# Kernel tuning notes

Measured on AMD Instinct MI355X. Metric: run time of the kernel, lower is better.

## Reference

```python
import math
import jax, jax.numpy as jnp
import numpy as np

B, C, E = 8, 2048, 1024

def setup_inputs() -> dict:
    key = jax.random.key(0)
    ks = jax.random.split(key, 7)
    s_e = 1.0 / math.sqrt(E)
    s_c = 1.0 / math.sqrt(C)
    return {
        'x': jax.random.normal(ks[0], (B, C, E), dtype=jnp.float32),
        'fc_w': jax.random.normal(ks[1], (E, E), dtype=jnp.float32) * s_e,
        'fc_b': jax.random.normal(ks[2], (E,), dtype=jnp.float32) * s_e,
        'alt_fc_w': jax.random.normal(ks[3], (C, C), dtype=jnp.float32) * s_c,
        'alt_fc_b': jax.random.normal(ks[4], (C,), dtype=jnp.float32) * s_c,
        'vfc_w': jax.random.normal(ks[5], (E, E), dtype=jnp.float32) * s_e,
        'vfc_b': jax.random.normal(ks[6], (E,), dtype=jnp.float32) * s_e,
    }

def reference(x, fc_w, fc_b, alt_fc_w, alt_fc_b, vfc_w, vfc_b):
    # y = fc(x): [b,c,e]
    y = jnp.einsum('bce,fe->bcf', x, fc_w) + fc_b
    # yx = alt_fc(x^T): [b,e,c] -> Linear over context dim -> [b,e,k]
    xx = jnp.swapaxes(x, 1, 2)                    # [b,e,c]
    yx = jnp.einsum('bec,kc->bek', xx, alt_fc_w) + alt_fc_b
    # attention scores: [b,c,k]
    attn = jnp.einsum('bce,bek->bck', y, yx)
    scale = 1.0 / math.sqrt(attn.shape[-1])
    attn = jax.nn.softmax(attn * scale, axis=-1)
    # values
    vx = jnp.einsum('bke,fe->bkf', x, vfc_w) + vfc_b
    out = jnp.einsum('bck,bke->bce', attn, vx)
    # post_feed=None -> return y only
    return out
```

## Files before the change

### kernel.cpp

```cpp
#include <hip/hip_runtime.h>
#include <stdint.h>

#define Bb 8
#define Cc 2048
#define Ee 1024

typedef unsigned short u16;
typedef __attribute__((ext_vector_type(8))) short short8;
typedef __attribute__((ext_vector_type(4))) float f32x4;

__device__ __forceinline__ u16 f2bf(float f){
    unsigned u = __builtin_bit_cast(unsigned, f);
    return (u16)((u + 0x7fffu + ((u >> 16) & 1u)) >> 16);
}
__device__ __forceinline__ float bf2f(u16 h){
    return __builtin_bit_cast(float, ((unsigned)h) << 16);
}
__device__ __forceinline__ void gld16(const void* g, void* l){
    __builtin_amdgcn_global_load_lds(
        (const __attribute__((address_space(1))) unsigned int*)g,
        (__attribute__((address_space(3))) unsigned int*)l,
        16, 0, 0);
}
#define MFMA(a,b,c) __builtin_amdgcn_mfma_f32_16x16x32_bf16((a),(b),(c),0,0,0)
#define SBAR()  __builtin_amdgcn_s_barrier()
#define SCHED0() __builtin_amdgcn_sched_barrier(0)
#define LGKM8() asm volatile("s_waitcnt lgkmcnt(8)" ::: "memory")
#define LGKM0() asm volatile("s_waitcnt lgkmcnt(0)" ::: "memory")
#define VMCNT0() asm volatile("s_waitcnt vmcnt(0)" ::: "memory")

__global__ __launch_bounds__(256) void k_cast(const float* __restrict__ s,
                                              u16* __restrict__ d, long n4){
    long i = (long)blockIdx.x * 256 + threadIdx.x;
    const long stride = (long)gridDim.x * 256;
    for (; i < n4; i += stride){
        float4 f = ((const float4*)s)[i];
        ushort4 o = make_ushort4(f2bf(f.x), f2bf(f.y), f2bf(f.z), f2bf(f.w));
        ((ushort4*)d)[i] = o;
    }
}

__global__ __launch_bounds__(256) void k_cast_xt(const float* __restrict__ src,
                                                 u16* __restrict__ xb,
                                                 u16* __restrict__ xbT){
    __shared__ float tile[32][33];
    const int b = blockIdx.z;
    src += (long)b * Cc * Ee;
    xb  += (long)b * Cc * Ee;
    xbT += (long)b * Cc * Ee;
    const int c0 = blockIdx.x * 32;
    const int r0 = blockIdx.y * 32;
    const int tx = threadIdx.x & 31;
    const int ty = threadIdx.x >> 5;
    #pragma unroll
    for (int p = 0; p < 4; ++p){
        float v = src[(long)(r0 + ty + p*8) * Ee + c0 + tx];
        tile[ty + p*8][tx] = v;
        xb[(long)(r0 + ty + p*8) * Ee + c0 + tx] = f2bf(v);
    }
    __syncthreads();
    #pragma unroll
    for (int p = 0; p < 4; ++p)
        xbT[(long)(c0 + ty + p*8) * Cc + r0 + tx] = f2bf(tile[tx][ty + p*8]);
}

template<int BIAS_MODE, int OUT_F32>
__global__ __launch_bounds__(256, 2)
void k_gemm128(const u16* __restrict__ A, const u16* __restrict__ Bm,
               void* __restrict__ Cout, const float* __restrict__ bias,
               int N, int K, long sA, long sB, long sC, float scale)
{
    __shared__ __attribute__((aligned(16))) char smem[65536];

    const int gx = gridDim.x, gy = gridDim.y;
    const int nwg = gx * gy * gridDim.z;
    const int lin = blockIdx.x + gx * (blockIdx.y + gy * blockIdx.z);
    const int swz = (lin & 7) * (nwg >> 3) + (lin >> 3);
    const int bx = swz % gx;
    const int tmp = swz / gx;
    const int by = tmp % gy;
    const int bz = tmp / gy;

    A  += (long)bz * sA;
    Bm += (long)bz * sB;
    u16*   Cm = (u16*)Cout + (OUT_F32 ? 0 : (long)bz * sC);
    float* Cf = (float*)Cout + (OUT_F32 ? (long)bz * sC : 0);

    const int tid  = threadIdx.x;
    const int lane = tid & 63;
    const int wave = tid >> 6;
    const int wr = wave >> 1;
    const int wc = wave & 1;
    const int tileM = bx * 128;
    const int tileN = by * 128;

    const int srow   = tid >> 3;
    const int schunk = (tid & 7) ^ (srow & 7);
    const u16* Ag = A  + (long)(tileM + srow) * K + schunk * 8;
    const u16* Bg = Bm + (long)(tileN + srow) * K + schunk * 8;
    const long uK = (long)32 * K;
    const int  ldst = tid * 16;

    const int lrow = lane & 15;
    const int lk   = lane >> 4;
    const int sw   = lrow & 7;
    const int cs0  = ((0 + lk) ^ sw) * 16;
    const int cs1  = ((4 + lk) ^ sw) * 16;
    const int arow0 = (wr*64 + lrow) * 128;
    const int brow0 = 16384 + (wc*64 + lrow) * 128;

    f32x4 acc[4][4];
    #pragma unroll
    for (int m = 0; m < 4; ++m)
        #pragma unroll
        for (int n = 0; n < 4; ++n)
            acc[m][n] = (f32x4){0.f,0.f,0.f,0.f};

    char* sm = smem;
    #pragma unroll
    for (int u = 0; u < 4; ++u) gld16(Ag + u*uK, sm + u*4096 + ldst);
    #pragma unroll
    for (int u = 0; u < 4; ++u) gld16(Bg + u*uK, sm + 16384 + u*4096 + ldst);
    __syncthreads();

    const int NT = K >> 6;
    short8 a0[4], b0[4], a1[4], b1[4];

    for (int t = 0; t < NT; ++t){
        const bool pref = (t + 1) < NT;
        char* cbuf = sm + ((t & 1) << 15);
        char* nbuf = sm + (((t + 1) & 1) << 15);
        const u16* Agt = Ag + (long)(t + 1) * 64;
        const u16* Bgt = Bg + (long)(t + 1) * 64;

        if (pref){
            gld16(Agt + 0*uK, nbuf + 0*4096 + ldst);
            gld16(Agt + 1*uK, nbuf + 1*4096 + ldst);
            gld16(Agt + 2*uK, nbuf + 2*4096 + ldst);
            gld16(Agt + 3*uK, nbuf + 3*4096 + ldst);
            gld16(Bgt + 0*uK, nbuf + 16384 + 0*4096 + ldst);
            gld16(Bgt + 1*uK, nbuf + 16384 + 1*4096 + ldst);
            gld16(Bgt + 2*uK, nbuf + 16384 + 2*4096 + ldst);
            gld16(Bgt + 3*uK, nbuf + 16384 + 3*4096 + ldst);
        }

        #pragma unroll
        for (int m = 0; m < 4; ++m) a0[m] = *(const short8*)(cbuf + arow0 + m*2048 + cs0);
        #pragma unroll
        for (int n = 0; n < 4; ++n) b0[n] = *(const short8*)(cbuf + brow0 + n*2048 + cs0);
        #pragma unroll
        for (int m = 0; m < 4; ++m) a1[m] = *(const short8*)(cbuf + arow0 + m*2048 + cs1);
        #pragma unroll
        for (int n = 0; n < 4; ++n) b1[n] = *(const short8*)(cbuf + brow0 + n*2048 + cs1);

        LGKM8(); SCHED0();
        __builtin_amdgcn_s_setprio(1);
        #pragma unroll
        for (int m = 0; m < 4; ++m)
            #pragma unroll
            for (int n = 0; n < 4; ++n)
                acc[m][n] = MFMA(a0[m], b0[n], acc[m][n]);
        __builtin_amdgcn_s_setprio(0);

        LGKM0(); SCHED0();
        __builtin_amdgcn_s_setprio(1);
        #pragma unroll
        for (int m = 0; m < 4; ++m)
            #pragma unroll
            for (int n = 0; n < 4; ++n)
                acc[m][n] = MFMA(a1[m], b1[n], acc[m][n]);
        __builtin_amdgcn_s_setprio(0);

        VMCNT0(); SBAR(); SCHED0();
    }

    const int r0base = tileM + wr*64 + lk*4;
    const int cbase  = tileN + wc*64 + lrow;
    #pragma unroll
    for (int m = 0; m < 4; ++m){
        const int r0 = r0base + m*16;
        #pragma unroll
        for (int n = 0; n < 4; ++n){
            const int c = cbase + n*16;
            f32x4 v = acc[m][n];
            #pragma unroll
            for (int j = 0; j < 4; ++j){
                float val = v[j] * scale;
                if (BIAS_MODE == 1) val += bias[c];
                if (BIAS_MODE == 2) val += bias[r0 + j];
                if (OUT_F32) Cf[(long)(r0 + j) * N + c] = val;
                else         Cm[(long)(r0 + j) * N + c] = f2bf(val);
            }
        }
    }
}

__global__ __launch_bounds__(256) void k_softmax(u16* __restrict__ P){
    u16* p = P + (long)blockIdx.x * Cc;
    const int tid = threadIdx.x;
    short8 raw = *(const short8*)(p + tid * 8);
    float v[8];
    float mx = -3.0e38f;
    #pragma unroll
    for (int i = 0; i < 8; ++i){ v[i] = bf2f((u16)raw[i]); mx = fmaxf(mx, v[i]); }
    #pragma unroll
    for (int o = 32; o > 0; o >>= 1) mx = fmaxf(mx, __shfl_xor(mx, o));
    __shared__ float redm[4];
    if ((tid & 63) == 0) redm[tid >> 6] = mx;
    __syncthreads();
    mx = fmaxf(fmaxf(redm[0], redm[1]), fmaxf(redm[2], redm[3]));
    float s = 0.f;
    #pragma unroll
    for (int i = 0; i < 8; ++i){ v[i] = __expf(v[i] - mx); s += v[i]; }
    #pragma unroll
    for (int o = 32; o > 0; o >>= 1) s += __shfl_xor(s, o);
    __shared__ float reds[4];
    if ((tid & 63) == 0) reds[tid >> 6] = s;
    __syncthreads();
    s = reds[0] + reds[1] + reds[2] + reds[3];
    const float inv = 1.f / s;
    short8 o8;
    #pragma unroll
    for (int i = 0; i < 8; ++i) o8[i] = (short)f2bf(v[i] * inv);
    *(short8*)(p + tid * 8) = o8;
}

static inline int cast_grid(long n4){
    long g = (n4 + 255) / 256;
    return (int)(g > 2048 ? 2048 : g);
}

extern "C" void kernel_launch(void* const* d_in, const int* in_sizes, int n_in,
                              void* d_out, int out_size, void* d_ws, size_t ws_size,
                              hipStream_t stream)
{
    const float* x     = (const float*)d_in[0];
    const float* fc_w  = (const float*)d_in[1];
    const float* fc_b  = (const float*)d_in[2];
    const float* altw  = (const float*)d_in[3];
    const float* altb  = (const float*)d_in[4];
    const float* vfc_w = (const float*)d_in[5];
    const float* vfc_b = (const float*)d_in[6];
    float* out = (float*)d_out;

    char* ws = (char*)d_ws;
    const size_t nBCE = (size_t)Bb * Cc * Ee;
    u16* xb   = (u16*)(ws);
    u16* xbT  = (u16*)(ws + 2 * nBCE);
    u16* P    = (u16*)(ws);
    u16* y    = (u16*)(ws + 4 * nBCE);
    u16* z    = (u16*)(ws + 6 * nBCE);
    u16* vxT  = (u16*)(ws + 8 * nBCE);
    u16* fcwb = (u16*)(ws + 10 * nBCE);
    u16* vfwb = fcwb + (size_t)Ee * Ee;
    u16* awb  = vfwb + (size_t)Ee * Ee;

    k_cast_xt<<<dim3(Ee / 32, Cc / 32, Bb), 256, 0, stream>>>(x, xb, xbT);
    k_cast<<<cast_grid((long)Ee * Ee / 4), 256, 0, stream>>>(fc_w, fcwb, (long)Ee * Ee / 4);
    k_cast<<<cast_grid((long)Ee * Ee / 4), 256, 0, stream>>>(vfc_w, vfwb, (long)Ee * Ee / 4);
    k_cast<<<cast_grid((long)Cc * Cc / 4), 256, 0, stream>>>(altw, awb, (long)Cc * Cc / 4);

    const long sBCE = (long)Cc * Ee;
    const long sBCC = (long)Cc * Cc;
    dim3 blk(256);

    k_gemm128<1, 0><<<dim3(Cc/128, Ee/128, Bb), blk, 0, stream>>>(
        xb, fcwb, y, fc_b, Ee, Ee, sBCE, 0, sBCE, 1.f);

    k_gemm128<2, 0><<<dim3(Ee/128, Cc/128, Bb), blk, 0, stream>>>(
        vfwb, xb, vxT, vfc_b, Cc, Ee, 0, sBCE, sBCE, 1.f);

    k_gemm128<2, 0><<<dim3(Cc/128, Ee/128, Bb), blk, 0, stream>>>(
        awb, xbT, z, altb, Ee, Cc, 0, sBCE, sBCE, 1.f);

    k_gemm128<0, 0><<<dim3(Cc/128, Cc/128, Bb), blk, 0, stream>>>(
        y, z, P, nullptr, Cc, Ee, sBCE, sBCE, sBCC, 0.022097086912079608f);

    k_softmax<<<Bb * Cc, 256, 0, stream>>>(P);

    k_gemm128<0, 1><<<dim3(Cc/128, Ee/128, Bb), blk, 0, stream>>>(
        P, vxT, out, nullptr, Ee, Cc, sBCC, sBCE, sBCE, 1.f);
}
```

Measured before the change: 358.0 us.

## Switch GEMMs to 128x256 tiles with K=32 steps and 1x4 wave layout

The GEMM kernel's output tile grows from 128x128 to 128x256. Each wave now covers all 128 rows and a 64-column strip, with 8x4 accumulators. The K step per iteration drops from 64 to 32, and the LDS layout is reswizzled so each 64-byte row chunk pair is packed into a 128-byte line. This is meant to raise arithmetic intensity per LDS/global byte and to reduce total LDS use to 48KB, at the cost of doubled accumulator registers (possible occupancy drop or spills under launch_bounds(256,2)), twice as many loop iterations and barriers, and half as many workgroups.

```diff
diff --git a/kernel.cpp b/kernel.cpp
--- a/kernel.cpp
+++ b/kernel.cpp
@@ -25,7 +25,7 @@
 #define MFMA(a,b,c) __builtin_amdgcn_mfma_f32_16x16x32_bf16((a),(b),(c),0,0,0)
 #define SBAR()  __builtin_amdgcn_s_barrier()
 #define SCHED0() __builtin_amdgcn_sched_barrier(0)
-#define LGKM8() asm volatile("s_waitcnt lgkmcnt(8)" ::: "memory")
+#define LGKM4() asm volatile("s_waitcnt lgkmcnt(4)" ::: "memory")
 #define LGKM0() asm volatile("s_waitcnt lgkmcnt(0)" ::: "memory")
 #define VMCNT0() asm volatile("s_waitcnt vmcnt(0)" ::: "memory")
 
@@ -66,11 +66,11 @@
 
 template<int BIAS_MODE, int OUT_F32>
 __global__ __launch_bounds__(256, 2)
-void k_gemm128(const u16* __restrict__ A, const u16* __restrict__ Bm,
+void k_gemm_bn(const u16* __restrict__ A, const u16* __restrict__ Bm,
                void* __restrict__ Cout, const float* __restrict__ bias,
                int N, int K, long sA, long sB, long sC, float scale)
 {
-    __shared__ __attribute__((aligned(16))) char smem[65536];
+    __shared__ __attribute__((aligned(16))) char smem[49152];
 
     const int gx = gridDim.x, gy = gridDim.y;
     const int nwg = gx * gy * gridDim.z;
@@ -88,100 +88,91 @@
 
     const int tid  = threadIdx.x;
     const int lane = tid & 63;
-    const int wave = tid >> 6;
-    const int wr = wave >> 1;
-    const int wc = wave & 1;
+    const int wc   = tid >> 6;
     const int tileM = bx * 128;
-    const int tileN = by * 128;
-
-    const int srow   = tid >> 3;
-    const int schunk = (tid & 7) ^ (srow & 7);
-    const u16* Ag = A  + (long)(tileM + srow) * K + schunk * 8;
-    const u16* Bg = Bm + (long)(tileN + srow) * K + schunk * 8;
-    const long uK = (long)32 * K;
+    const int tileN = by * 256;
+
+    const int lr_  = tid >> 3;
+    const int lc_  = (tid & 7) ^ (lr_ & 7);
+    const int trow = lr_ * 2 + (lc_ >> 2);
+    const int kch  = lc_ & 3;
+    const u16* Agp = A  + (long)(tileM + trow) * K + kch * 8;
+    const u16* Bgp = Bm + (long)(tileN + trow) * K + kch * 8;
+    const long uK = (long)64 * K;
     const int  ldst = tid * 16;
 
     const int lrow = lane & 15;
     const int lk   = lane >> 4;
-    const int sw   = lrow & 7;
-    const int cs0  = ((0 + lk) ^ sw) * 16;
-    const int cs1  = ((4 + lk) ^ sw) * 16;
-    const int arow0 = (wr*64 + lrow) * 128;
-    const int brow0 = 16384 + (wc*64 + lrow) * 128;
-
-    f32x4 acc[4][4];
-    #pragma unroll
-    for (int m = 0; m < 4; ++m)
+    const int roff = (lrow >> 1) * 128 + (((((lrow & 1) << 2) | lk) ^ ((lrow >> 1) & 7)) << 4);
+    const int aoff = roff;
+    const int boff = 8192 + wc * 4096 + roff;
+
+    f32x4 acc[8][4];
+    #pragma unroll
+    for (int m = 0; m < 8; ++m)
         #pragma unroll
         for (int n = 0; n < 4; ++n)
             acc[m][n] = (f32x4){0.f,0.f,0.f,0.f};
 
     char* sm = smem;
     #pragma unroll
-    for (int u = 0; u < 4; ++u) gld16(Ag + u*uK, sm + u*4096 + ldst);
-    #pragma unroll
-    for (int u = 0; u < 4; ++u) gld16(Bg + u*uK, sm + 16384 + u*4096 + ldst);
-    __syncthreads();
-
-    const int NT = K >> 6;
-    short8 a0[4], b0[4], a1[4], b1[4];
+    for (int u = 0; u < 2; ++u) gld16(Agp + u*uK, sm + u*4096 + ldst);
+    #pragma unroll
+    for (int u = 0; u < 4; ++u) gld16(Bgp + u*uK, sm + 8192 + u*4096 + ldst);
+    __syncthreads();
+
+    const int NT = K >> 5;
+    short8 aF[8], bF[4];
 
     for (int t = 0; t < NT; ++t){
         const bool pref = (t + 1) < NT;
-        char* cbuf = sm + ((t & 1) << 15);
-        char* nbuf = sm + (((t + 1) & 1) << 15);
-        const u16* Agt = Ag + (long)(t + 1) * 64;
-        const u16* Bgt = Bg + (long)(t + 1) * 64;
+        char* cbuf = sm + (t & 1) * 24576;
+        char* nbuf = sm + ((t + 1) & 1) * 24576;
+        const long g1 = (long)(t + 1) * 32;
 
         if (pref){
-            gld16(Agt + 0*uK, nbuf + 0*4096 + ldst);
-            gld16(Agt + 1*uK, nbuf + 1*4096 + ldst);
-            gld16(Agt + 2*uK, nbuf + 2*4096 + ldst);
-            gld16(Agt + 3*uK, nbuf + 3*4096 + ldst);
-            gld16(Bgt + 0*uK, nbuf + 16384 + 0*4096 + ldst);
-            gld16(Bgt + 1*uK, nbuf + 16384 + 1*4096 + ldst);
-            gld16(Bgt + 2*uK, nbuf + 16384 + 2*4096 + ldst);
-            gld16(Bgt + 3*uK, nbuf + 16384 + 3*4096 + ldst);
+            gld16(Agp + g1 + 0*uK, nbuf + 0*4096 + ldst);
+            gld16(Agp + g1 + 1*uK, nbuf + 1*4096 + ldst);
+            gld16(Bgp + g1 + 0*uK, nbuf + 8192 + 0*4096 + ldst);
+            gld16(Bgp + g1 + 1*uK, nbuf + 8192 + 1*4096 + ldst);
+            gld16(Bgp + g1 + 2*uK, nbuf + 8192 + 2*4096 + ldst);
+            gld16(Bgp + g1 + 3*4096/4096*uK*1, nbuf + 8192 + 3*4096 + ldst);
         }
 
         #pragma unroll
-        for (int m = 0; m < 4; ++m) a0[m] = *(const short8*)(cbuf + arow0 + m*2048 + cs0);
-        #pragma unroll
-        for (int n = 0; n < 4; ++n) b0[n] = *(const short8*)(cbuf + brow0 + n*2048 + cs0);
-        #pragma unroll
-        for (int m = 0; m < 4; ++m) a1[m] = *(const short8*)(cbuf + arow0 + m*2048 + cs1);
-        #pragma unroll
-        for (int n = 0; n < 4; ++n) b1[n] = *(const short8*)(cbuf + brow0 + n*2048 + cs1);
-
-        LGKM8(); SCHED0();
+        for (int n = 0; n < 4; ++n) bF[n] = *(const short8*)(cbuf + boff + n*1024);
+        #pragma unroll
+        for (int m = 0; m < 8; ++m) aF[m] = *(const short8*)(cbuf + aoff + m*1024);
+
+        LGKM4(); SCHED0();
         __builtin_amdgcn_s_setprio(1);
         #pragma unroll
         for (int m = 0; m < 4; ++m)
             #pragma unroll
             for (int n = 0; n < 4; ++n)
-                acc[m][n] = MFMA(a0[m], b0[n], acc[m][n]);
+                acc[m][n] = MFMA(aF[m], bF[n], acc[m][n]);
         __builtin_amdgcn_s_setprio(0);
 
         LGKM0(); SCHED0();
         __builtin_amdgcn_s_setprio(1);
         #pragma unroll
-        for (int m = 0; m < 4; ++m)
+        for (int m = 4; m < 8; ++m)
             #pragma unroll
             for (int n = 0; n < 4; ++n)
-                acc[m][n] = MFMA(a1[m], b1[n], acc[m][n]);
+                acc[m][n] = MFMA(aF[m], bF[n], acc[m][n]);
         __builtin_amdgcn_s_setprio(0);
 
         VMCNT0(); SBAR(); SCHED0();
     }
 
-    const int r0base = tileM + wr*64 + lk*4;
-    const int cbase  = tileN + wc*64 + lrow;
-    #pragma unroll
-    for (int m = 0; m < 4; ++m){
-        const int r0 = r0base + m*16;
+    const int r0base = tileM + lk * 4;
+    const int cbase  = tileN + wc * 64 + lrow;
+    #pragma unroll
+    for (int m = 0; m < 8; ++m){
+        const int r0 = r0base + m * 16;
         #pragma unroll
         for (int n = 0; n < 4; ++n){
-            const int c = cbase + n*16;
+            const int c = cbase + n * 16;
             f32x4 v = acc[m][n];
             #pragma unroll
             for (int j = 0; j < 4; ++j){
@@ -264,20 +255,20 @@
     const long sBCC = (long)Cc * Cc;
     dim3 blk(256);
 
-    k_gemm128<1, 0><<<dim3(Cc/128, Ee/128, Bb), blk, 0, stream>>>(
+    k_gemm_bn<1, 0><<<dim3(Cc/128, Ee/256, Bb), blk, 0, stream>>>(
         xb, fcwb, y, fc_b, Ee, Ee, sBCE, 0, sBCE, 1.f);
 
-    k_gemm128<2, 0><<<dim3(Ee/128, Cc/128, Bb), blk, 0, stream>>>(
+    k_gemm_bn<2, 0><<<dim3(Ee/128, Cc/256, Bb), blk, 0, stream>>>(
         vfwb, xb, vxT, vfc_b, Cc, Ee, 0, sBCE, sBCE, 1.f);
 
-    k_gemm128<2, 0><<<dim3(Cc/128, Ee/128, Bb), blk, 0, stream>>>(
+    k_gemm_bn<2, 0><<<dim3(Cc/128, Ee/256, Bb), blk, 0, stream>>>(
         awb, xbT, z, altb, Ee, Cc, 0, sBCE, sBCE, 1.f);
 
-    k_gemm128<0, 0><<<dim3(Cc/128, Cc/128, Bb), blk, 0, stream>>>(
+    k_gemm_bn<0, 0><<<dim3(Cc/128, Cc/256, Bb), blk, 0, stream>>>(
         y, z, P, nullptr, Cc, Ee, sBCE, sBCE, sBCC, 0.022097086912079608f);
 
     k_softmax<<<Bb * Cc, 256, 0, stream>>>(P);
 
-    k_gemm128<0, 1><<<dim3(Cc/128, Ee/128, Bb), blk, 0, stream>>>(
+    k_gemm_bn<0, 1><<<dim3(Cc/128, Ee/256, Bb), blk, 0, stream>>>(
         P, vxT, out, nullptr, Ee, Cc, sBCC, sBCE, sBCE, 1.f);
 }
```

Result: slower. 369.8 us (+3.3%).
